# Optimization experiments

Hardware: AMD Instinct MI355X
Metric: run time of the kernel (lower is better)

Reference implementation:

```python
import jax, jax.numpy as jnp
import numpy as np

B, N, I, J = 8, 2048, 64, 32
DA, DB = 64, 16
SCALE = DA ** -0.5


def setup_inputs() -> dict:
    key = jax.random.key(0)
    ks = jax.random.split(key, 9)
    s = lambda fan_in: 1.0 / np.sqrt(fan_in)
    return {
        "voxel_code": jax.random.normal(ks[0], (B, N, I, DA), jnp.float32),
        "trans_code": jax.random.normal(ks[1], (B, N, J, DB), jnp.float32),
        # linear weights stored as (in, out); PyTorch computes x @ W.T, equivalent math
        "Wq": jax.random.uniform(ks[2], (DA, DA), jnp.float32, -s(DA), s(DA)),
        "Wk": jax.random.uniform(ks[3], (DB, DA), jnp.float32, -s(DB), s(DB)),
        "Wv": jax.random.uniform(ks[4], (DB, DA), jnp.float32, -s(DB), s(DB)),
        "Wo": jax.random.uniform(ks[5], (DA, DA), jnp.float32, -s(DA), s(DA)),
        "bo": jax.random.uniform(ks[6], (DA,), jnp.float32, -s(DA), s(DA)),
        "ln_g": jnp.ones((DA,), jnp.float32),
        "ln_b": jnp.zeros((DA,), jnp.float32),
    }


def _layer_norm(x, g, b, eps=1e-5):
    mu = jnp.mean(x, axis=-1, keepdims=True)
    var = jnp.mean(jnp.square(x - mu), axis=-1, keepdims=True)
    return (x - mu) * jax.lax.rsqrt(var + eps) * g + b


def reference(voxel_code, trans_code, Wq, Wk, Wv, Wo, bo, ln_g, ln_b):
    q = jnp.einsum("bnid,de->bnie", voxel_code, Wq)        # [B,N,I,DA]
    k = jnp.einsum("bnjd,de->bnje", trans_code, Wk)        # [B,N,J,DA]
    v = jnp.einsum("bnjd,de->bnje", trans_code, Wv)        # [B,N,J,DA]
    attn = jax.nn.softmax(jnp.einsum("bnie,bnje->bnij", q, k) * SCALE, axis=-1)
    o = jnp.einsum("bnij,bnje->bnie", attn, v) + voxel_code  # residual
    # to_out: Linear -> Dropout(eval: identity) -> LayerNorm(eps=1e-5)
    return _layer_norm(o @ Wo + bo, ln_g, ln_b)
```

## Files before the change

kernel.cpp:

```cpp
#include <hip/hip_runtime.h>
#include <hip/hip_bf16.h>
#include <stdint.h>

typedef __attribute__((ext_vector_type(8))) __bf16 bf16x8;
typedef __attribute__((ext_vector_type(4))) __bf16 bf16x4;
typedef __attribute__((ext_vector_type(4))) float f32x4;
typedef __attribute__((ext_vector_type(4))) unsigned int u32x4;

#define MFMA16(a,b,c) __builtin_amdgcn_mfma_f32_16x16x32_bf16((a),(b),(c),0,0,0)

#define BATCH 8
#define NPTS  2048

__device__ __forceinline__ int swz128(int row, int col) {
    return row*128 + ((col*2) ^ (((row + (row >> 3)) & 7) << 4));
}
__device__ __forceinline__ int swz64(int row, int col) {
    return row*64 + ((col*2) ^ (((row + (row >> 2)) & 3) << 4));
}
__device__ __forceinline__ __bf16* p128(char* base, int row, int col) {
    return (__bf16*)(base + swz128(row, col));
}
__device__ __forceinline__ __bf16* p64(char* base, int row, int col) {
    return (__bf16*)(base + swz64(row, col));
}
__device__ __forceinline__ bf16x8 ld8_128(char* base, int row, int col) {
    return *(const bf16x8*)p128(base, row, col);
}
__device__ __forceinline__ bf16x8 ld8_64(char* base, int row, int col) {
    return *(const bf16x8*)p64(base, row, col);
}

__global__ void prep_weights(const float* __restrict__ Wq, const float* __restrict__ Wk,
                             const float* __restrict__ Wv, const float* __restrict__ Wo,
                             __bf16* __restrict__ ws)
{
    int idx = blockIdx.x * 256 + threadIdx.x;
    char* wsb = (char*)ws;
    if (idx < 4096) {
        int n = idx >> 6, k = idx & 63;
        *(__bf16*)(wsb + swz128(n, k)) = (__bf16)Wo[k*64 + n];
    } else if (idx < 6144) {
        int i = idx - 4096, f = i >> 5, db = i & 31;
        float acc = 0.f;
        if (db < 16) {
            for (int e = 0; e < 64; ++e) acc += Wv[db*64 + e] * Wo[e*64 + f];
        }
        *(__bf16*)(wsb + 8192 + swz64(f, db)) = (__bf16)acc;
    } else if (idx < 7168) {
        int i = idx - 6144, db = i >> 6, d = i & 63;
        float acc = 0.f;
        for (int e = 0; e < 64; ++e) acc += Wq[d*64 + e] * Wk[db*64 + e];
        *(__bf16*)(wsb + 12288 + db*128 + d*2) = (__bf16)(acc * 0.125f);
    }
}

__global__ void __launch_bounds__(256, 6) xattn_kernel(
    const float* __restrict__ voxel, const float* __restrict__ trans,
    const float* __restrict__ ws,
    const float* __restrict__ bo, const float* __restrict__ lng,
    const float* __restrict__ lnb, float* __restrict__ out)
{
    __shared__ __align__(16) char lds[24576];
    char* Wot = lds;
    char* W2t = lds + 8192;
    char* Xb  = lds + 12288;
    char* XPb = lds + 20480;

    const int tid = threadIdx.x;
    const int bn  = blockIdx.x;
    const int w   = tid >> 6;
    const int l   = tid & 63;
    const int l15 = l & 15;
    const int lq  = l >> 4;

    const f32x4 fzero = {0.f, 0.f, 0.f, 0.f};

    bf16x8 mf0, mf1, tfrag[2], ttf;
    {
        const char* wsb = (const char*)ws;
        u32x4 wimg[3];
        #pragma unroll
        for (int i = 0; i < 3; ++i)
            wimg[i] = *(const u32x4*)(wsb + i*4096 + tid*16);
        #pragma unroll
        for (int i = 0; i < 3; ++i)
            *(u32x4*)(lds + i*4096 + tid*16) = wimg[i];
        mf0 = *(const bf16x8*)(wsb + 12288 + l15*128 + lq*16);
        mf1 = *(const bf16x8*)(wsb + 12288 + l15*128 + 64 + lq*16);
        #pragma unroll
        for (int i = 0; i < 8; ++i) { tfrag[0][i] = (__bf16)0.f; tfrag[1][i] = (__bf16)0.f; }
        if (lq < 2) {
            #pragma unroll
            for (int tj = 0; tj < 2; ++tj) {
                const f32x4* gT = (const f32x4*)(trans + (size_t)bn*512 + (16*tj + l15)*16 + lq*8);
                f32x4 u0 = gT[0], u1 = gT[1];
                #pragma unroll
                for (int i = 0; i < 4; ++i) {
                    tfrag[tj][i]     = (__bf16)u0[i];
                    tfrag[tj][i + 4] = (__bf16)u1[i];
                }
            }
        }
        {
            const float* gT = trans + (size_t)bn * 512;
            float tt[8];
            #pragma unroll
            for (int i = 0; i < 8; ++i) tt[i] = gT[(lq*8 + i)*16 + l15];
            #pragma unroll
            for (int i = 0; i < 8; ++i) ttf[i] = (__bf16)tt[i];
        }
        const f32x4* gX = (const f32x4*)(voxel + (size_t)bn * 4096);
        #pragma unroll
        for (int j = 0; j < 4; ++j) {
            f32x4 v = gX[j*256 + tid];
            int gi  = j*256 + tid;
            int row = gi >> 4;
            int col = (gi & 15) * 4;
            bf16x4 h;
            #pragma unroll
            for (int i = 0; i < 4; ++i) h[i] = (__bf16)v[i];
            *(bf16x4*)p128(Xb, row, col) = h;
        }
        if (tid < 128) {
            f32x4 z = {0.f, 0.f, 0.f, 0.f};
            *(f32x4*)p64(XPb, tid >> 1, 16 + (tid & 1)*8) = z;
        }
    }
    asm volatile("s_waitcnt vmcnt(0) lgkmcnt(0)" ::: "memory");
    __syncthreads();

    bf16x8 xa0 = ld8_128(Xb, 16*w + l15, lq*8);
    bf16x8 xa1 = ld8_128(Xb, 16*w + l15, 32 + lq*8);

    {
        f32x4 xm = MFMA16(xa0, mf0, fzero);
        xm = MFMA16(xa1, mf1, xm);
        #pragma unroll
        for (int r = 0; r < 4; ++r)
            *p64(XPb, 16*w + lq*4 + r, l15) = (__bf16)xm[r];
    }
    {
        bf16x8 xma = ld8_64(XPb, 16*w + l15, lq*8);
        f32x4 s0 = MFMA16(xma, tfrag[0], fzero);
        f32x4 s1 = MFMA16(xma, tfrag[1], fzero);
        #pragma unroll
        for (int r = 0; r < 4; ++r) {
            float p0 = __expf(s0[r]);
            float p1 = __expf(s1[r]);
            float su = p0 + p1;
            #pragma unroll
            for (int off = 1; off < 16; off <<= 1) su += __shfl_xor(su, off);
            float inv = __builtin_amdgcn_rcpf(su);
            *p64(XPb, 16*w + lq*4 + r, l15)      = (__bf16)(p0 * inv);
            *p64(XPb, 16*w + lq*4 + r, 16 + l15) = (__bf16)(p1 * inv);
        }
    }
    {
        bf16x8 ap = ld8_64(XPb, 16*w + l15, lq*8);
        f32x4 pt = MFMA16(ap, ttf, fzero);
        #pragma unroll
        for (int r = 0; r < 4; ++r) {
            *p64(XPb, 16*w + lq*4 + r, l15)      = (__bf16)pt[r];
            *p64(XPb, 16*w + lq*4 + r, 16 + l15) = (__bf16)0.f;
        }
    }
    f32x4 y[4];
    {
        bf16x8 pta = ld8_64(XPb, 16*w + l15, lq*8);
        #pragma unroll
        for (int t = 0; t < 4; ++t) {
            bf16x8 b0  = ld8_128(Wot, 16*t + l15, lq*8);
            bf16x8 b1  = ld8_128(Wot, 16*t + l15, 32 + lq*8);
            bf16x8 w2b = ld8_64 (W2t, 16*t + l15, lq*8);
            y[t] = MFMA16(xa0, b0, fzero);
            y[t] = MFMA16(xa1, b1, y[t]);
            y[t] = MFMA16(pta, w2b, y[t]);
        }
    }
    __syncthreads();
    {
        float bo4[4], g4[4], b4[4];
        #pragma unroll
        for (int t = 0; t < 4; ++t) {
            int c = 16*t + l15;
            bo4[t] = bo[c]; g4[t] = lng[c]; b4[t] = lnb[c];
        }
        float* Ybuf = (float*)lds;
        #pragma unroll
        for (int r = 0; r < 4; ++r) {
            float v0 = y[0][r] + bo4[0];
            float v1 = y[1][r] + bo4[1];
            float v2 = y[2][r] + bo4[2];
            float v3 = y[3][r] + bo4[3];
            float s1 = v0 + v1 + v2 + v3;
            float s2 = v0*v0 + v1*v1 + v2*v2 + v3*v3;
            #pragma unroll
            for (int off = 1; off < 16; off <<= 1) {
                s1 += __shfl_xor(s1, off);
                s2 += __shfl_xor(s2, off);
            }
            float mu  = s1 * 0.015625f;
            float var = s2 * 0.015625f - mu * mu;
            float rs  = rsqrtf(var + 1e-5f);
            float* yrow = Ybuf + (16*w + lq*4 + r) * 68;
            yrow[     l15] = (v0 - mu) * rs * g4[0] + b4[0];
            yrow[16 + l15] = (v1 - mu) * rs * g4[1] + b4[1];
            yrow[32 + l15] = (v2 - mu) * rs * g4[2] + b4[2];
            yrow[48 + l15] = (v3 - mu) * rs * g4[3] + b4[3];
        }
        float* gout = out + (size_t)bn * 4096;
        #pragma unroll
        for (int s = 0; s < 4; ++s) {
            int row = 16*w + 4*s + (l >> 4);
            f32x4 v = *(const f32x4*)(Ybuf + row*68 + (l & 15)*4);
            *(f32x4*)(gout + row*64 + (l & 15)*4) = v;
        }
    }
}

extern "C" void kernel_launch(void* const* d_in, const int* in_sizes, int n_in,
                              void* d_out, int out_size, void* d_ws, size_t ws_size,
                              hipStream_t stream) {
    const float* voxel = (const float*)d_in[0];
    const float* trans = (const float*)d_in[1];
    const float* Wq = (const float*)d_in[2];
    const float* Wk = (const float*)d_in[3];
    const float* Wv = (const float*)d_in[4];
    const float* Wo = (const float*)d_in[5];
    const float* bo = (const float*)d_in[6];
    const float* g  = (const float*)d_in[7];
    const float* b  = (const float*)d_in[8];
    float* o = (float*)d_out;

    prep_weights<<<dim3(28), dim3(256), 0, stream>>>(Wq, Wk, Wv, Wo, (__bf16*)d_ws);
    xattn_kernel<<<dim3(BATCH * NPTS), dim3(256), 0, stream>>>(
        voxel, trans, (const float*)d_ws, bo, g, b, o);
}
```

Before: 121.2 us.

## Process two (b,n) points per block and transpose MFMA operand order

Each block now handles two points instead of one. This halves the grid and spreads the per-block cost of staging the weight tiles into LDS over twice the work. MFMA operands are swapped so results come out transposed, which lets intermediates be stored as packed bf16x4 writes and reduces the softmax reduction to two cross-lane shuffles. In exchange, LDS use rises to 36 KB, the launch-bounds occupancy hint drops from 6 to 4, and register pressure grows from holding two sets of fragments.

```diff
diff --git a/kernel.cpp b/kernel.cpp
--- a/kernel.cpp
+++ b/kernel.cpp
@@ -11,6 +11,7 @@
 
 #define BATCH 8
 #define NPTS  2048
+#define GRID  (BATCH * NPTS / 2)
 
 __device__ __forceinline__ int swz128(int row, int col) {
     return row*128 + ((col*2) ^ (((row + (row >> 3)) & 7) << 4));
@@ -55,20 +56,20 @@
     }
 }
 
-__global__ void __launch_bounds__(256, 6) xattn_kernel(
+__global__ void __launch_bounds__(256, 4) xattn_kernel(
     const float* __restrict__ voxel, const float* __restrict__ trans,
     const float* __restrict__ ws,
     const float* __restrict__ bo, const float* __restrict__ lng,
     const float* __restrict__ lnb, float* __restrict__ out)
 {
-    __shared__ __align__(16) char lds[24576];
+    __shared__ __align__(16) char lds[36864];
     char* Wot = lds;
     char* W2t = lds + 8192;
-    char* Xb  = lds + 12288;
-    char* XPb = lds + 20480;
+    #define XBQ(q)  (lds + 12288 + (q)*8192)
+    #define XPQ(q)  (lds + 28672 + (q)*4096)
 
     const int tid = threadIdx.x;
-    const int bn  = blockIdx.x;
+    const int bn0 = blockIdx.x * 2;
     const int w   = tid >> 6;
     const int l   = tid & 63;
     const int l15 = l & 15;
@@ -76,7 +77,7 @@
 
     const f32x4 fzero = {0.f, 0.f, 0.f, 0.f};
 
-    bf16x8 mf0, mf1, tfrag[2], ttf;
+    bf16x8 mf0, mf1, tfrag0[2], tfrag1[2], ttf0, ttf1;
     {
         const char* wsb = (const char*)ws;
         u32x4 wimg[3];
@@ -89,93 +90,131 @@
         mf0 = *(const bf16x8*)(wsb + 12288 + l15*128 + lq*16);
         mf1 = *(const bf16x8*)(wsb + 12288 + l15*128 + 64 + lq*16);
         #pragma unroll
-        for (int i = 0; i < 8; ++i) { tfrag[0][i] = (__bf16)0.f; tfrag[1][i] = (__bf16)0.f; }
-        if (lq < 2) {
-            #pragma unroll
-            for (int tj = 0; tj < 2; ++tj) {
-                const f32x4* gT = (const f32x4*)(trans + (size_t)bn*512 + (16*tj + l15)*16 + lq*8);
-                f32x4 u0 = gT[0], u1 = gT[1];
-                #pragma unroll
-                for (int i = 0; i < 4; ++i) {
-                    tfrag[tj][i]     = (__bf16)u0[i];
-                    tfrag[tj][i + 4] = (__bf16)u1[i];
+        for (int q = 0; q < 2; ++q) {
+            const int bn = bn0 + q;
+            bf16x8* tf = (q == 0) ? tfrag0 : tfrag1;
+            #pragma unroll
+            for (int i = 0; i < 8; ++i) { tf[0][i] = (__bf16)0.f; tf[1][i] = (__bf16)0.f; }
+            if (lq < 2) {
+                #pragma unroll
+                for (int tj = 0; tj < 2; ++tj) {
+                    const f32x4* gT = (const f32x4*)(trans + (size_t)bn*512 + (16*tj + l15)*16 + lq*8);
+                    f32x4 u0 = gT[0], u1 = gT[1];
+                    #pragma unroll
+                    for (int i = 0; i < 4; ++i) {
+                        tf[tj][i]     = (__bf16)u0[i];
+                        tf[tj][i + 4] = (__bf16)u1[i];
+                    }
                 }
             }
+            {
+                const float* gT = trans + (size_t)bn * 512;
+                float tt[8];
+                #pragma unroll
+                for (int i = 0; i < 8; ++i) tt[i] = gT[(lq*8 + i)*16 + l15];
+                bf16x8 tv;
+                #pragma unroll
+                for (int i = 0; i < 8; ++i) tv[i] = (__bf16)tt[i];
+                if (q == 0) ttf0 = tv; else ttf1 = tv;
+            }
+            const f32x4* gX = (const f32x4*)(voxel + (size_t)bn * 4096);
+            #pragma unroll
+            for (int j = 0; j < 4; ++j) {
+                f32x4 v = gX[j*256 + tid];
+                int gi  = j*256 + tid;
+                int row = gi >> 4;
+                int col = (gi & 15) * 4;
+                bf16x4 h;
+                #pragma unroll
+                for (int i = 0; i < 4; ++i) h[i] = (__bf16)v[i];
+                *(bf16x4*)p128(XBQ(q), row, col) = h;
+            }
         }
         {
-            const float* gT = trans + (size_t)bn * 512;
-            float tt[8];
-            #pragma unroll
-            for (int i = 0; i < 8; ++i) tt[i] = gT[(lq*8 + i)*16 + l15];
-            #pragma unroll
-            for (int i = 0; i < 8; ++i) ttf[i] = (__bf16)tt[i];
-        }
-        const f32x4* gX = (const f32x4*)(voxel + (size_t)bn * 4096);
-        #pragma unroll
-        for (int j = 0; j < 4; ++j) {
-            f32x4 v = gX[j*256 + tid];
-            int gi  = j*256 + tid;
-            int row = gi >> 4;
-            int col = (gi & 15) * 4;
-            bf16x4 h;
-            #pragma unroll
-            for (int i = 0; i < 4; ++i) h[i] = (__bf16)v[i];
-            *(bf16x4*)p128(Xb, row, col) = h;
-        }
-        if (tid < 128) {
+            int q  = tid >> 7;
+            int t2 = tid & 127;
             f32x4 z = {0.f, 0.f, 0.f, 0.f};
-            *(f32x4*)p64(XPb, tid >> 1, 16 + (tid & 1)*8) = z;
+            *(f32x4*)p64(XPQ(q), t2 >> 1, 16 + (t2 & 1)*8) = z;
         }
     }
     asm volatile("s_waitcnt vmcnt(0) lgkmcnt(0)" ::: "memory");
     __syncthreads();
 
-    bf16x8 xa0 = ld8_128(Xb, 16*w + l15, lq*8);
-    bf16x8 xa1 = ld8_128(Xb, 16*w + l15, 32 + lq*8);
-
-    {
-        f32x4 xm = MFMA16(xa0, mf0, fzero);
-        xm = MFMA16(xa1, mf1, xm);
-        #pragma unroll
-        for (int r = 0; r < 4; ++r)
-            *p64(XPb, 16*w + lq*4 + r, l15) = (__bf16)xm[r];
-    }
-    {
-        bf16x8 xma = ld8_64(XPb, 16*w + l15, lq*8);
-        f32x4 s0 = MFMA16(xma, tfrag[0], fzero);
-        f32x4 s1 = MFMA16(xma, tfrag[1], fzero);
+    bf16x8 xa00 = ld8_128(XBQ(0), 16*w + l15, lq*8);
+    bf16x8 xa01 = ld8_128(XBQ(0), 16*w + l15, 32 + lq*8);
+    bf16x8 xa10 = ld8_128(XBQ(1), 16*w + l15, lq*8);
+    bf16x8 xa11 = ld8_128(XBQ(1), 16*w + l15, 32 + lq*8);
+
+    {
+        f32x4 xm0 = MFMA16(mf0, xa00, fzero);
+        xm0 = MFMA16(mf1, xa01, xm0);
+        f32x4 xm1 = MFMA16(mf0, xa10, fzero);
+        xm1 = MFMA16(mf1, xa11, xm1);
+        bf16x4 h0, h1;
+        #pragma unroll
+        for (int r = 0; r < 4; ++r) { h0[r] = (__bf16)xm0[r]; h1[r] = (__bf16)xm1[r]; }
+        *(bf16x4*)p64(XPQ(0), 16*w + l15, lq*4) = h0;
+        *(bf16x4*)p64(XPQ(1), 16*w + l15, lq*4) = h1;
+    }
+    {
+        bf16x8 xma0 = ld8_64(XPQ(0), 16*w + l15, lq*8);
+        bf16x8 xma1 = ld8_64(XPQ(1), 16*w + l15, lq*8);
+        f32x4 sa0 = MFMA16(tfrag0[0], xma0, fzero);
+        f32x4 sa1 = MFMA16(tfrag0[1], xma0, fzero);
+        f32x4 sb0 = MFMA16(tfrag1[0], xma1, fzero);
+        f32x4 sb1 = MFMA16(tfrag1[1], xma1, fzero);
+        float pa0[4], pa1[4], pb0[4], pb1[4];
+        float sua = 0.f, sub = 0.f;
         #pragma unroll
         for (int r = 0; r < 4; ++r) {
-            float p0 = __expf(s0[r]);
-            float p1 = __expf(s1[r]);
-            float su = p0 + p1;
-            #pragma unroll
-            for (int off = 1; off < 16; off <<= 1) su += __shfl_xor(su, off);
-            float inv = __builtin_amdgcn_rcpf(su);
-            *p64(XPb, 16*w + lq*4 + r, l15)      = (__bf16)(p0 * inv);
-            *p64(XPb, 16*w + lq*4 + r, 16 + l15) = (__bf16)(p1 * inv);
-        }
-    }
-    {
-        bf16x8 ap = ld8_64(XPb, 16*w + l15, lq*8);
-        f32x4 pt = MFMA16(ap, ttf, fzero);
+            pa0[r] = __expf(sa0[r]); pa1[r] = __expf(sa1[r]);
+            pb0[r] = __expf(sb0[r]); pb1[r] = __expf(sb1[r]);
+            sua += pa0[r] + pa1[r];
+            sub += pb0[r] + pb1[r];
+        }
+        sua += __shfl_xor(sua, 16); sub += __shfl_xor(sub, 16);
+        sua += __shfl_xor(sua, 32); sub += __shfl_xor(sub, 32);
+        float inva = __builtin_amdgcn_rcpf(sua);
+        float invb = __builtin_amdgcn_rcpf(sub);
+        bf16x4 ha0, ha1, hb0, hb1;
         #pragma unroll
         for (int r = 0; r < 4; ++r) {
-            *p64(XPb, 16*w + lq*4 + r, l15)      = (__bf16)pt[r];
-            *p64(XPb, 16*w + lq*4 + r, 16 + l15) = (__bf16)0.f;
-        }
-    }
-    f32x4 y[4];
-    {
-        bf16x8 pta = ld8_64(XPb, 16*w + l15, lq*8);
+            ha0[r] = (__bf16)(pa0[r] * inva);
+            ha1[r] = (__bf16)(pa1[r] * inva);
+            hb0[r] = (__bf16)(pb0[r] * invb);
+            hb1[r] = (__bf16)(pb1[r] * invb);
+        }
+        *(bf16x4*)p64(XPQ(0), 16*w + l15, lq*4)      = ha0;
+        *(bf16x4*)p64(XPQ(0), 16*w + l15, 16 + lq*4) = ha1;
+        *(bf16x4*)p64(XPQ(1), 16*w + l15, lq*4)      = hb0;
+        *(bf16x4*)p64(XPQ(1), 16*w + l15, 16 + lq*4) = hb1;
+    }
+    {
+        bf16x8 ap0 = ld8_64(XPQ(0), 16*w + l15, lq*8);
+        bf16x8 ap1 = ld8_64(XPQ(1), 16*w + l15, lq*8);
+        f32x4 pt0 = MFMA16(ttf0, ap0, fzero);
+        f32x4 pt1 = MFMA16(ttf1, ap1, fzero);
+        bf16x4 h0, h1;
+        #pragma unroll
+        for (int r = 0; r < 4; ++r) { h0[r] = (__bf16)pt0[r]; h1[r] = (__bf16)pt1[r]; }
+        *(bf16x4*)p64(XPQ(0), 16*w + l15, lq*4) = h0;
+        *(bf16x4*)p64(XPQ(1), 16*w + l15, lq*4) = h1;
+    }
+    f32x4 y0[4], y1[4];
+    {
+        bf16x8 pta0 = ld8_64(XPQ(0), 16*w + l15, lq*8);
+        bf16x8 pta1 = ld8_64(XPQ(1), 16*w + l15, lq*8);
         #pragma unroll
         for (int t = 0; t < 4; ++t) {
             bf16x8 b0  = ld8_128(Wot, 16*t + l15, lq*8);
             bf16x8 b1  = ld8_128(Wot, 16*t + l15, 32 + lq*8);
             bf16x8 w2b = ld8_64 (W2t, 16*t + l15, lq*8);
-            y[t] = MFMA16(xa0, b0, fzero);
-            y[t] = MFMA16(xa1, b1, y[t]);
-            y[t] = MFMA16(pta, w2b, y[t]);
+            y0[t] = MFMA16(xa00, b0, fzero);
+            y0[t] = MFMA16(xa01, b1, y0[t]);
+            y0[t] = MFMA16(pta0, w2b, y0[t]);
+            y1[t] = MFMA16(xa10, b0, fzero);
+            y1[t] = MFMA16(xa11, b1, y1[t]);
+            y1[t] = MFMA16(pta1, w2b, y1[t]);
         }
     }
     __syncthreads();
@@ -186,37 +225,42 @@
             int c = 16*t + l15;
             bo4[t] = bo[c]; g4[t] = lng[c]; b4[t] = lnb[c];
         }
-        float* Ybuf = (float*)lds;
-        #pragma unroll
-        for (int r = 0; r < 4; ++r) {
-            float v0 = y[0][r] + bo4[0];
-            float v1 = y[1][r] + bo4[1];
-            float v2 = y[2][r] + bo4[2];
-            float v3 = y[3][r] + bo4[3];
-            float s1 = v0 + v1 + v2 + v3;
-            float s2 = v0*v0 + v1*v1 + v2*v2 + v3*v3;
-            #pragma unroll
-            for (int off = 1; off < 16; off <<= 1) {
-                s1 += __shfl_xor(s1, off);
-                s2 += __shfl_xor(s2, off);
-            }
-            float mu  = s1 * 0.015625f;
-            float var = s2 * 0.015625f - mu * mu;
-            float rs  = rsqrtf(var + 1e-5f);
-            float* yrow = Ybuf + (16*w + lq*4 + r) * 68;
-            yrow[     l15] = (v0 - mu) * rs * g4[0] + b4[0];
-            yrow[16 + l15] = (v1 - mu) * rs * g4[1] + b4[1];
-            yrow[32 + l15] = (v2 - mu) * rs * g4[2] + b4[2];
-            yrow[48 + l15] = (v3 - mu) * rs * g4[3] + b4[3];
-        }
-        float* gout = out + (size_t)bn * 4096;
-        #pragma unroll
-        for (int s = 0; s < 4; ++s) {
-            int row = 16*w + 4*s + (l >> 4);
-            f32x4 v = *(const f32x4*)(Ybuf + row*68 + (l & 15)*4);
-            *(f32x4*)(gout + row*64 + (l & 15)*4) = v;
-        }
-    }
+        #pragma unroll
+        for (int q = 0; q < 2; ++q) {
+            float* Ybuf = (float*)(lds + q*17408);
+            #pragma unroll
+            for (int r = 0; r < 4; ++r) {
+                float v0 = ((q == 0) ? y0[0][r] : y1[0][r]) + bo4[0];
+                float v1 = ((q == 0) ? y0[1][r] : y1[1][r]) + bo4[1];
+                float v2 = ((q == 0) ? y0[2][r] : y1[2][r]) + bo4[2];
+                float v3 = ((q == 0) ? y0[3][r] : y1[3][r]) + bo4[3];
+                float s1 = v0 + v1 + v2 + v3;
+                float s2 = v0*v0 + v1*v1 + v2*v2 + v3*v3;
+                #pragma unroll
+                for (int off = 1; off < 16; off <<= 1) {
+                    s1 += __shfl_xor(s1, off);
+                    s2 += __shfl_xor(s2, off);
+                }
+                float mu  = s1 * 0.015625f;
+                float var = s2 * 0.015625f - mu * mu;
+                float rs  = rsqrtf(var + 1e-5f);
+                float* yrow = Ybuf + (16*w + lq*4 + r) * 68;
+                yrow[     l15] = (v0 - mu) * rs * g4[0] + b4[0];
+                yrow[16 + l15] = (v1 - mu) * rs * g4[1] + b4[1];
+                yrow[32 + l15] = (v2 - mu) * rs * g4[2] + b4[2];
+                yrow[48 + l15] = (v3 - mu) * rs * g4[3] + b4[3];
+            }
+            float* gout = out + (size_t)(bn0 + q) * 4096;
+            #pragma unroll
+            for (int s = 0; s < 4; ++s) {
+                int row = 16*w + 4*s + (l >> 4);
+                f32x4 v = *(const f32x4*)(Ybuf + row*68 + (l & 15)*4);
+                *(f32x4*)(gout + row*64 + (l & 15)*4) = v;
+            }
+        }
+    }
+    #undef XBQ
+    #undef XPQ
 }
 
 extern "C" void kernel_launch(void* const* d_in, const int* in_sizes, int n_in,
@@ -234,6 +278,6 @@
     float* o = (float*)d_out;
 
     prep_weights<<<dim3(28), dim3(256), 0, stream>>>(Wq, Wk, Wv, Wo, (__bf16*)d_ws);
-    xattn_kernel<<<dim3(BATCH * NPTS), dim3(256), 0, stream>>>(
+    xattn_kernel<<<dim3(GRID), dim3(256), 0, stream>>>(
         voxel, trans, (const float*)d_ws, bo, g, b, o);
 }
```

Result: faster. 117.7 us (-2.9%).
